# Kernel tuning notes

Hardware: AMD Instinct MI355X
Metric: run time of the kernel (lower is better)

The kernel has to match this reference:

```python
import jax, jax.numpy as jnp
import numpy as np

HIDDEN = 2048
N_HEADS = 16
N_KV_HEADS = 4
HEAD_DIM = HIDDEN // N_HEADS  # 128
ROPE_THETA = 10000.0
BATCH = 2
SEQ = 2048


def setup_inputs() -> dict:
    key = jax.random.key(0)
    k1, k2, k3, k4, k5 = jax.random.split(key, 5)
    s = 0.02
    return {
        "hidden_states": jax.random.normal(k1, (BATCH, SEQ, HIDDEN), dtype=jnp.float32),
        "attention_mask": jnp.zeros((BATCH, 1, 1, SEQ), dtype=jnp.float32),
        "Wq": jax.random.normal(k2, (HIDDEN, N_HEADS * HEAD_DIM), dtype=jnp.float32) * s,
        "Wk": jax.random.normal(k3, (HIDDEN, N_KV_HEADS * HEAD_DIM), dtype=jnp.float32) * s,
        "Wv": jax.random.normal(k4, (HIDDEN, N_KV_HEADS * HEAD_DIM), dtype=jnp.float32) * s,
        "Wo": jax.random.normal(k5, (N_HEADS * HEAD_DIM, HIDDEN), dtype=jnp.float32) * s,
    }


def _rope_cos_sin(seq_len, dtype):
    inv_freq = 1.0 / (ROPE_THETA ** (jnp.arange(0, HEAD_DIM, 2, dtype=jnp.float32) / HEAD_DIM))
    t = jnp.arange(seq_len, dtype=jnp.float32)
    freqs = t[:, None] * inv_freq[None, :]            # [S, D/2]
    emb = jnp.concatenate([freqs, freqs], axis=-1)    # [S, D]
    cos = jnp.cos(emb)[None, None, :, :].astype(dtype)  # [1,1,S,D]
    sin = jnp.sin(emb)[None, None, :, :].astype(dtype)
    return cos, sin


def _apply_rope(x, cos, sin):
    # x: [B,H,S,D]; faithful to torch code: rotated = cat((-x[...,1::2], x[...,::2]), -1)
    x1 = x[..., ::2]
    x2 = x[..., 1::2]
    rotated = jnp.concatenate([-x2, x1], axis=-1)
    return x * cos + rotated * sin


def reference(hidden_states, attention_mask, Wq, Wk, Wv, Wo):
    B, S, _ = hidden_states.shape
    scale = HEAD_DIM ** -0.5

    q = (hidden_states @ Wq).reshape(B, S, N_HEADS, HEAD_DIM).transpose(0, 2, 1, 3)      # [B,H,S,D]
    k = (hidden_states @ Wk).reshape(B, S, N_KV_HEADS, HEAD_DIM).transpose(0, 2, 1, 3)   # [B,KV,S,D]
    v = (hidden_states @ Wv).reshape(B, S, N_KV_HEADS, HEAD_DIM).transpose(0, 2, 1, 3)

    cos, sin = _rope_cos_sin(S, hidden_states.dtype)
    q = _apply_rope(q, cos, sin)
    k = _apply_rope(k, cos, sin)

    rep = N_HEADS // N_KV_HEADS
    k = jnp.repeat(k, rep, axis=1)  # [B,H,S,D]
    v = jnp.repeat(v, rep, axis=1)

    scores = jnp.einsum("bhqd,bhkd->bhqk", q, k) * scale  # [B,H,S,S]
    causal = jnp.tril(jnp.ones((S, S), dtype=bool))[None, None]
    scores = jnp.where(causal, scores, -jnp.inf)
    scores = scores + attention_mask  # additive float mask, broadcast [B,1,1,S]

    attn = jax.nn.softmax(scores, axis=-1)
    out = jnp.einsum("bhqk,bhkd->bhqd", attn, v)           # [B,H,S,D]
    out = out.transpose(0, 2, 1, 3).reshape(B, S, N_HEADS * HEAD_DIM)
    return out @ Wo
```

## Files before the change

### kernel.cpp

```cpp
#include <hip/hip_runtime.h>
#include <hip/hip_bf16.h>

#define BATCH 2
#define SEQ   2048
#define NH    16
#define NKV   4
#define HD    128
#define KDIM  2048
#define MROWS 4096
#define NQKV  3072

typedef __attribute__((ext_vector_type(8))) short  s16x8;
typedef __attribute__((ext_vector_type(4))) short  s16x4;
typedef __attribute__((ext_vector_type(4))) float  f32x4;
typedef __attribute__((ext_vector_type(8))) __bf16 b16x8;

__device__ __forceinline__ unsigned short f2bf(float f) {
  __hip_bfloat16 h = __float2bfloat16(f);
  return *reinterpret_cast<unsigned short*>(&h);
}
__device__ __forceinline__ float bf2f(unsigned short h) {
  union { unsigned int u; float f; } x; x.u = ((unsigned int)h) << 16;
  return x.f;
}

__device__ __forceinline__ f32x4 MFMA16(s16x8 a, s16x8 b, f32x4 c) {
  return __builtin_amdgcn_mfma_f32_16x16x32_bf16(
      __builtin_bit_cast(b16x8, a), __builtin_bit_cast(b16x8, b), c, 0, 0, 0);
}

__device__ __forceinline__ void gload_lds16(const void* g, void* lds) {
  __builtin_amdgcn_global_load_lds(
      (const __attribute__((address_space(1))) void*)g,
      (__attribute__((address_space(3))) void*)lds, 16, 0, 0);
}

__global__ __launch_bounds__(256) void transpose_convert(
    const float* __restrict__ W, unsigned short* __restrict__ WT, int Kd, int Nd) {
  __shared__ float tile[32][33];
  int n0 = blockIdx.x * 32, k0 = blockIdx.y * 32;
  int tx = threadIdx.x & 31, ty = threadIdx.x >> 5;
#pragma unroll
  for (int i = 0; i < 4; ++i)
    tile[ty + i * 8][tx] = W[(size_t)(k0 + ty + i * 8) * Nd + n0 + tx];
  __syncthreads();
#pragma unroll
  for (int i = 0; i < 4; ++i)
    WT[(size_t)(n0 + ty + i * 8) * Kd + k0 + tx] = f2bf(tile[tx][ty + i * 8]);
}

__global__ __launch_bounds__(256) void conv_bf16(
    const float* __restrict__ X, unsigned short* __restrict__ Y) {
  int i = blockIdx.x * 256 + threadIdx.x;
  const float4 a = ((const float4*)X)[2 * i];
  const float4 b = ((const float4*)X)[2 * i + 1];
  s16x8 o;
  o[0] = (short)f2bf(a.x); o[1] = (short)f2bf(a.y);
  o[2] = (short)f2bf(a.z); o[3] = (short)f2bf(a.w);
  o[4] = (short)f2bf(b.x); o[5] = (short)f2bf(b.y);
  o[6] = (short)f2bf(b.z); o[7] = (short)f2bf(b.w);
  ((s16x8*)Y)[i] = o;
}

__global__ __launch_bounds__(256) void rope_table_kernel(float* __restrict__ tbl) {
  int i = blockIdx.x * 256 + threadIdx.x;
  int s = i >> 6, j = i & 63;
  float inv = powf(10000.0f, -(float)(2 * j) * (1.0f / 128.0f));
  float f = (float)s * inv;
  tbl[2 * i]     = cosf(f);
  tbl[2 * i + 1] = sinf(f);
}

__global__ __launch_bounds__(256) void gemm_qkv(
    const unsigned short* __restrict__ A, const unsigned short* __restrict__ BT,
    unsigned short* __restrict__ Qo, unsigned short* __restrict__ Ko,
    unsigned short* __restrict__ Vo) {
  __shared__ __align__(16) unsigned short la[128][32];
  __shared__ __align__(16) unsigned short lb[128][32];
  int tid = threadIdx.x, lane = tid & 63, w = tid >> 6;
  int m0 = blockIdx.y * 128, n0 = blockIdx.x * 128;
  int wr = (w >> 1) * 64, wc = (w & 1) * 64;
  int fr = lane & 15, kg = (lane >> 4) * 8, rg = (lane >> 4) * 4;
  f32x4 acc[4][4] = {};
  for (int kt = 0; kt < KDIM; kt += 32) {
    __syncthreads();
#pragma unroll
    for (int i = 0; i < 2; ++i) {
      int idx = tid + i * 256;
      int row = idx >> 2, seg = idx & 3;
      gload_lds16(A + (size_t)(m0 + row) * KDIM + kt + seg * 8,
                  (char*)la + (size_t)(i * 256 + w * 64) * 16);
      gload_lds16(BT + (size_t)(n0 + row) * KDIM + kt + seg * 8,
                  (char*)lb + (size_t)(i * 256 + w * 64) * 16);
    }
    __syncthreads();
    s16x8 af[4], bf[4];
#pragma unroll
    for (int mi = 0; mi < 4; ++mi) af[mi] = *(const s16x8*)(&la[wr + mi * 16 + fr][kg]);
#pragma unroll
    for (int ni = 0; ni < 4; ++ni) bf[ni] = *(const s16x8*)(&lb[wc + ni * 16 + fr][kg]);
#pragma unroll
    for (int mi = 0; mi < 4; ++mi)
#pragma unroll
      for (int ni = 0; ni < 4; ++ni) acc[mi][ni] = MFMA16(af[mi], bf[ni], acc[mi][ni]);
  }
  int rbase = m0 + wr + rg;
#pragma unroll
  for (int ni = 0; ni < 4; ++ni) {
    int gn = n0 + wc + ni * 16 + fr;
    if (gn < 2048) {
      int hh = gn >> 7, d = gn & 127;
#pragma unroll
      for (int mi = 0; mi < 4; ++mi)
#pragma unroll
        for (int r = 0; r < 4; ++r) {
          int grow = rbase + mi * 16 + r;
          int bb = grow >> 11, ss = grow & 2047;
          Qo[((size_t)(bb * NH + hh) * SEQ + ss) * HD + d] = f2bf(acc[mi][ni][r]);
        }
    } else if (gn < 2560) {
      int c = gn - 2048, kvh = c >> 7, d = c & 127;
#pragma unroll
      for (int mi = 0; mi < 4; ++mi)
#pragma unroll
        for (int r = 0; r < 4; ++r) {
          int grow = rbase + mi * 16 + r;
          int bb = grow >> 11, ss = grow & 2047;
          Ko[((size_t)(bb * NKV + kvh) * SEQ + ss) * HD + d] = f2bf(acc[mi][ni][r]);
        }
    } else {
      int c = gn - 2560, kvh = c >> 7, d = c & 127;
#pragma unroll
      for (int mi = 0; mi < 4; ++mi) {
        int grow0 = rbase + mi * 16;
        int bb = grow0 >> 11, ss = grow0 & 2047;
        s16x4 pk;
#pragma unroll
        for (int r = 0; r < 4; ++r) pk[r] = (short)f2bf(acc[mi][ni][r]);
        *(s16x4*)(Vo + ((size_t)(bb * NKV + kvh) * HD + d) * SEQ + ss) = pk;
      }
    }
  }
}

__global__ __launch_bounds__(256) void gemm_out(
    const unsigned short* __restrict__ A, const unsigned short* __restrict__ BT,
    float* __restrict__ C) {
  __shared__ __align__(16) unsigned short la[128][32];
  __shared__ __align__(16) unsigned short lb[128][32];
  int tid = threadIdx.x, lane = tid & 63, w = tid >> 6;
  int m0 = blockIdx.y * 128, n0 = blockIdx.x * 128;
  int wr = (w >> 1) * 64, wc = (w & 1) * 64;
  int fr = lane & 15, kg = (lane >> 4) * 8, rg = (lane >> 4) * 4;
  f32x4 acc[4][4] = {};
  for (int kt = 0; kt < KDIM; kt += 32) {
    __syncthreads();
#pragma unroll
    for (int i = 0; i < 2; ++i) {
      int idx = tid + i * 256;
      int row = idx >> 2, seg = idx & 3;
      gload_lds16(A + (size_t)(m0 + row) * KDIM + kt + seg * 8,
                  (char*)la + (size_t)(i * 256 + w * 64) * 16);
      gload_lds16(BT + (size_t)(n0 + row) * KDIM + kt + seg * 8,
                  (char*)lb + (size_t)(i * 256 + w * 64) * 16);
    }
    __syncthreads();
    s16x8 af[4], bf[4];
#pragma unroll
    for (int mi = 0; mi < 4; ++mi) af[mi] = *(const s16x8*)(&la[wr + mi * 16 + fr][kg]);
#pragma unroll
    for (int ni = 0; ni < 4; ++ni) bf[ni] = *(const s16x8*)(&lb[wc + ni * 16 + fr][kg]);
#pragma unroll
    for (int mi = 0; mi < 4; ++mi)
#pragma unroll
      for (int ni = 0; ni < 4; ++ni) acc[mi][ni] = MFMA16(af[mi], bf[ni], acc[mi][ni]);
  }
  int rbase = m0 + wr + rg;
#pragma unroll
  for (int ni = 0; ni < 4; ++ni) {
    int gn = n0 + wc + ni * 16 + fr;
#pragma unroll
    for (int mi = 0; mi < 4; ++mi)
#pragma unroll
      for (int r = 0; r < 4; ++r)
        C[(size_t)(rbase + mi * 16 + r) * 2048 + gn] = acc[mi][ni][r];
  }
}

__global__ __launch_bounds__(256) void rope2(
    unsigned short* __restrict__ X, const float* __restrict__ tbl) {
  __shared__ __align__(16) unsigned short xs[32][136];
  int tid = threadIdx.x;
  size_t r0 = (size_t)blockIdx.x * 32;
#pragma unroll
  for (int i = 0; i < 2; ++i) {
    int idx = tid + i * 256;
    int pr = idx >> 4, seg = idx & 15;
    *(s16x8*)(&xs[pr][seg * 8]) = *(const s16x8*)(X + (r0 + pr) * 128 + seg * 8);
  }
  __syncthreads();
  int pr = tid >> 3, jb = (tid & 7) * 8;
  size_t row = r0 + pr;
  int s = (int)(row & (SEQ - 1));
  s16x8 o0, o1;
#pragma unroll
  for (int j0 = 0; j0 < 8; ++j0) {
    int j = jb + j0;
    float c  = tbl[(s * 64 + j) * 2];
    float sn = tbl[(s * 64 + j) * 2 + 1];
    float xj   = bf2f(xs[pr][j]);
    float xj64 = bf2f(xs[pr][j + 64]);
    float x2j  = bf2f(xs[pr][2 * j]);
    float x2j1 = bf2f(xs[pr][2 * j + 1]);
    o0[j0] = (short)f2bf(xj * c - x2j1 * sn);
    o1[j0] = (short)f2bf(xj64 * c + x2j * sn);
  }
  unsigned short* xp = X + row * 128;
  *(s16x8*)(xp + jb)      = o0;
  *(s16x8*)(xp + 64 + jb) = o1;
}

__global__ __launch_bounds__(256, 2) void attn_fwd(
    const unsigned short* __restrict__ Q, const unsigned short* __restrict__ K,
    const unsigned short* __restrict__ VT, const float* __restrict__ mask,
    unsigned short* __restrict__ O) {
  __shared__ __align__(16) unsigned short kt_[2][64][136];
  __shared__ __align__(16) unsigned short vt_[128][72];
  __shared__ __align__(16) unsigned short pt_[4][32][40];

  int tid = threadIdx.x, lane = tid & 63, w = tid >> 6;
  int l = blockIdx.x;
  int grp = l & 7, slot = l >> 3;
  int hloc = slot & 3, qt = 15 - (slot >> 2);
  int b = grp >> 2, kvh = grp & 3, h = kvh * 4 + hloc;
  int qbase = qt * 128;
  int fr = lane & 15, g = lane >> 4, kg = g * 8, rg = g * 4;
  int qw = qbase + w * 32;

  const unsigned short* Qb = Q + (size_t)(b * NH + h) * SEQ * HD;
  const unsigned short* Kb = K + (size_t)(b * NKV + kvh) * SEQ * HD;
  const unsigned short* Vb = VT + (size_t)(b * NKV + kvh) * HD * SEQ;
  const float* mb = mask + (size_t)b * SEQ;

  s16x8 aq[2][4];
#pragma unroll
  for (int nq = 0; nq < 2; ++nq)
#pragma unroll
    for (int dc = 0; dc < 4; ++dc)
      aq[nq][dc] = *(const s16x8*)(Qb + (size_t)(qw + nq * 16 + fr) * HD + dc * 32 + kg);

  int krow = tid >> 4, kpos = (tid & 15) * 8;

  f32x4 oacc[2][8] = {};
  float m_r[2] = {-3e38f, -3e38f}, l_r[2] = {0.f, 0.f};
  const float sc = 0.08838834764831845f;
  int ntiles = 2 * qt + 2;

  s16x8 kreg[4], vreg[4];
#pragma unroll
  for (int i = 0; i < 4; ++i)
    kreg[i] = *(const s16x8*)(Kb + (size_t)(krow + i * 16) * HD + kpos);
#pragma unroll
  for (int i = 0; i < 4; ++i) {
    int c = tid + 256 * i;
    vreg[i] = *(const s16x8*)(Vb + (size_t)(c >> 3) * SEQ + (c & 7) * 8);
  }
#pragma unroll
  for (int i = 0; i < 4; ++i)
    *(s16x8*)(&kt_[0][krow + i * 16][kpos]) = kreg[i];
  __syncthreads();

  int cur = 0;
  for (int t = 0; t < ntiles; ++t) {
    int kv0 = t * 64;
    bool active = (kv0 <= qw + 31);

#pragma unroll
    for (int i = 0; i < 4; ++i) {
      int c = tid + 256 * i;
      *(s16x8*)(&vt_[c >> 3][(c & 7) * 8]) = vreg[i];
    }
    if (t + 1 < ntiles) {
#pragma unroll
      for (int i = 0; i < 4; ++i)
        kreg[i] = *(const s16x8*)(Kb + (size_t)(kv0 + 64 + krow + i * 16) * HD + kpos);
    }

    f32x4 sf[4][2];
    if (active) {
      __builtin_amdgcn_s_setprio(1);
#pragma unroll
      for (int mk = 0; mk < 4; ++mk) {
        s16x8 ak[4];
#pragma unroll
        for (int dc = 0; dc < 4; ++dc)
          ak[dc] = *(const s16x8*)(&kt_[cur][mk * 16 + fr][dc * 32 + kg]);
        sf[mk][0] = f32x4{0.f, 0.f, 0.f, 0.f};
        sf[mk][1] = f32x4{0.f, 0.f, 0.f, 0.f};
#pragma unroll
        for (int nq = 0; nq < 2; ++nq)
#pragma unroll
          for (int dc = 0; dc < 4; ++dc)
            sf[mk][nq] = MFMA16(ak[dc], aq[nq][dc], sf[mk][nq]);
      }
      __builtin_amdgcn_s_setprio(0);

#pragma unroll
      for (int mk = 0; mk < 4; ++mk) {
        float4 mv = *(const float4*)(mb + kv0 + mk * 16 + rg);
        float mvr[4] = {mv.x, mv.y, mv.z, mv.w};
#pragma unroll
        for (int nq = 0; nq < 2; ++nq)
#pragma unroll
          for (int r = 0; r < 4; ++r) {
            int kv = kv0 + mk * 16 + rg + r;
            int q  = qw + nq * 16 + fr;
            float v = sf[mk][nq][r] * sc + mvr[r];
            sf[mk][nq][r] = (kv <= q) ? v : -3e38f;
          }
      }

#pragma unroll
      for (int nq = 0; nq < 2; ++nq) {
        float pm = -3e38f;
#pragma unroll
        for (int mk = 0; mk < 4; ++mk)
#pragma unroll
          for (int r = 0; r < 4; ++r) pm = fmaxf(pm, sf[mk][nq][r]);
        pm = fmaxf(pm, __shfl_xor(pm, 16, 64));
        pm = fmaxf(pm, __shfl_xor(pm, 32, 64));
        if (!__all(pm - m_r[nq] <= 8.0f)) {
          float mo = m_r[nq];
          float mn = fmaxf(mo, pm);
          float al = __expf(mo - mn);
          m_r[nq] = mn;
          l_r[nq] *= al;
#pragma unroll
          for (int r = 0; r < 4; ++r) {
            float ar = __shfl(al, rg + r, 16);
#pragma unroll
            for (int od = 0; od < 8; ++od) oacc[nq][od][r] *= ar;
          }
        }
        float rs = 0.f;
#pragma unroll
        for (int mk = 0; mk < 4; ++mk)
#pragma unroll
          for (int r = 0; r < 4; ++r) {
            float p = __expf(sf[mk][nq][r] - m_r[nq]);
            sf[mk][nq][r] = p;
            rs += p;
          }
        rs += __shfl_xor(rs, 16, 64);
        rs += __shfl_xor(rs, 32, 64);
        l_r[nq] += rs;
      }
    }

    if (t + 1 < ntiles) {
#pragma unroll
      for (int i = 0; i < 4; ++i)
        *(s16x8*)(&kt_[cur ^ 1][krow + i * 16][kpos]) = kreg[i];
    }
    __syncthreads();

    if (t + 1 < ntiles) {
#pragma unroll
      for (int i = 0; i < 4; ++i) {
        int c = tid + 256 * i;
        vreg[i] = *(const s16x8*)(Vb + (size_t)(c >> 3) * SEQ + kv0 + 64 + (c & 7) * 8);
      }
    }
    if (active) {
#pragma unroll
      for (int kk = 0; kk < 2; ++kk) {
#pragma unroll
        for (int nq = 0; nq < 2; ++nq)
#pragma unroll
          for (int mh = 0; mh < 2; ++mh) {
            int mk = kk * 2 + mh;
            s16x4 pk;
#pragma unroll
            for (int r = 0; r < 4; ++r) pk[r] = (short)f2bf(sf[mk][nq][r]);
            *(s16x4*)(&pt_[w][nq * 16 + fr][mh * 16 + rg]) = pk;
          }
        s16x8 ap[2];
#pragma unroll
        for (int nq = 0; nq < 2; ++nq)
          ap[nq] = *(const s16x8*)(&pt_[w][nq * 16 + fr][kg]);
        __builtin_amdgcn_s_setprio(1);
#pragma unroll
        for (int od = 0; od < 8; ++od) {
          s16x8 bv = *(const s16x8*)(&vt_[od * 16 + fr][kk * 32 + kg]);
#pragma unroll
          for (int nq = 0; nq < 2; ++nq)
            oacc[nq][od] = MFMA16(ap[nq], bv, oacc[nq][od]);
        }
        __builtin_amdgcn_s_setprio(0);
      }
    }
    __syncthreads();
    cur ^= 1;
  }

  int bS = b * SEQ;
#pragma unroll
  for (int nq = 0; nq < 2; ++nq) {
    float iv = 1.0f / l_r[nq];
    float ivr[4];
#pragma unroll
    for (int r = 0; r < 4; ++r) ivr[r] = __shfl(iv, rg + r, 16);
#pragma unroll
    for (int r = 0; r < 4; ++r) {
      unsigned short* op = O + (size_t)(bS + qw + nq * 16 + rg + r) * 2048 + h * 128 + fr;
#pragma unroll
      for (int od = 0; od < 8; ++od)
        op[od * 16] = f2bf(oacc[nq][od][r] * ivr[r]);
    }
  }
}

extern "C" void kernel_launch(void* const* d_in, const int* in_sizes, int n_in,
                              void* d_out, int out_size, void* d_ws, size_t ws_size,
                              hipStream_t stream) {
  const float* hidden = (const float*)d_in[0];
  const float* mask   = (const float*)d_in[1];
  const float* Wq     = (const float*)d_in[2];
  const float* Wk     = (const float*)d_in[3];
  const float* Wv     = (const float*)d_in[4];
  const float* Wo     = (const float*)d_in[5];
  float* out = (float*)d_out;

  char* ws = (char*)d_ws;
  unsigned short* BT  = (unsigned short*)(ws);
  unsigned short* WoT = (unsigned short*)(ws + 12582912);
  unsigned short* Qb  = (unsigned short*)(ws + 20971520);
  unsigned short* Kb  = (unsigned short*)(ws + 37748736);
  unsigned short* VT  = (unsigned short*)(ws + 41943040);
  unsigned short* AO  = (unsigned short*)(ws + 46137344);
  float*          tbl = (float*)(ws + 62914560);
  unsigned short* Ab  = AO;

  conv_bf16<<<MROWS * KDIM / (256 * 8), 256, 0, stream>>>(hidden, Ab);
  transpose_convert<<<dim3(64, 64), 256, 0, stream>>>(Wq, BT, KDIM, 2048);
  transpose_convert<<<dim3(16, 64), 256, 0, stream>>>(Wk, BT + (size_t)2048 * KDIM, KDIM, 512);
  transpose_convert<<<dim3(16, 64), 256, 0, stream>>>(Wv, BT + (size_t)2560 * KDIM, KDIM, 512);
  transpose_convert<<<dim3(64, 64), 256, 0, stream>>>(Wo, WoT, KDIM, 2048);
  rope_table_kernel<<<512, 256, 0, stream>>>(tbl);

  gemm_qkv<<<dim3(NQKV / 128, MROWS / 128), 256, 0, stream>>>(Ab, BT, Qb, Kb, VT);
  rope2<<<(BATCH * NH * SEQ) / 32, 256, 0, stream>>>(Qb, tbl);
  rope2<<<(BATCH * NKV * SEQ) / 32, 256, 0, stream>>>(Kb, tbl);
  attn_fwd<<<dim3(512), 256, 0, stream>>>(Qb, Kb, VT, mask, AO);
  gemm_out<<<dim3(2048 / 128, MROWS / 128), 256, 0, stream>>>(AO, WoT, out);
}
```

Baseline: 234.6 us.

## Shrink attention query tile to 64, read V directly from global, use exp2

```diff
diff --git a/kernel.cpp b/kernel.cpp
--- a/kernel.cpp
+++ b/kernel.cpp
@@ -220,51 +220,44 @@
   *(s16x8*)(xp + 64 + jb) = o1;
 }
 
-__global__ __launch_bounds__(256, 2) void attn_fwd(
+__global__ __launch_bounds__(256, 4) void attn_fwd(
     const unsigned short* __restrict__ Q, const unsigned short* __restrict__ K,
     const unsigned short* __restrict__ VT, const float* __restrict__ mask,
     unsigned short* __restrict__ O) {
   __shared__ __align__(16) unsigned short kt_[2][64][136];
-  __shared__ __align__(16) unsigned short vt_[128][72];
-  __shared__ __align__(16) unsigned short pt_[4][32][40];
+  __shared__ __align__(16) unsigned short pt_[4][16][36];
 
   int tid = threadIdx.x, lane = tid & 63, w = tid >> 6;
   int l = blockIdx.x;
   int grp = l & 7, slot = l >> 3;
-  int hloc = slot & 3, qt = 15 - (slot >> 2);
+  int hloc = slot & 3, qt = 31 - (slot >> 2);
   int b = grp >> 2, kvh = grp & 3, h = kvh * 4 + hloc;
-  int qbase = qt * 128;
+  int qbase = qt * 64;
   int fr = lane & 15, g = lane >> 4, kg = g * 8, rg = g * 4;
-  int qw = qbase + w * 32;
+  int qw = qbase + w * 16;
 
   const unsigned short* Qb = Q + (size_t)(b * NH + h) * SEQ * HD;
   const unsigned short* Kb = K + (size_t)(b * NKV + kvh) * SEQ * HD;
   const unsigned short* Vb = VT + (size_t)(b * NKV + kvh) * HD * SEQ;
   const float* mb = mask + (size_t)b * SEQ;
 
-  s16x8 aq[2][4];
-#pragma unroll
-  for (int nq = 0; nq < 2; ++nq)
-#pragma unroll
-    for (int dc = 0; dc < 4; ++dc)
-      aq[nq][dc] = *(const s16x8*)(Qb + (size_t)(qw + nq * 16 + fr) * HD + dc * 32 + kg);
+  s16x8 aq[4];
+#pragma unroll
+  for (int dc = 0; dc < 4; ++dc)
+    aq[dc] = *(const s16x8*)(Qb + (size_t)(qw + fr) * HD + dc * 32 + kg);
 
   int krow = tid >> 4, kpos = (tid & 15) * 8;
 
-  f32x4 oacc[2][8] = {};
-  float m_r[2] = {-3e38f, -3e38f}, l_r[2] = {0.f, 0.f};
-  const float sc = 0.08838834764831845f;
-  int ntiles = 2 * qt + 2;
-
-  s16x8 kreg[4], vreg[4];
+  f32x4 oacc[8] = {};
+  float m_r = -3e38f, l_r = 0.f;
+  const float sc2 = 0.12751744584812722f;
+  const float L2E = 1.44269504088896f;
+  int ntiles = qt + 1;
+
+  s16x8 kreg[4];
 #pragma unroll
   for (int i = 0; i < 4; ++i)
     kreg[i] = *(const s16x8*)(Kb + (size_t)(krow + i * 16) * HD + kpos);
-#pragma unroll
-  for (int i = 0; i < 4; ++i) {
-    int c = tid + 256 * i;
-    vreg[i] = *(const s16x8*)(Vb + (size_t)(c >> 3) * SEQ + (c & 7) * 8);
-  }
 #pragma unroll
   for (int i = 0; i < 4; ++i)
     *(s16x8*)(&kt_[0][krow + i * 16][kpos]) = kreg[i];
@@ -273,20 +266,16 @@
   int cur = 0;
   for (int t = 0; t < ntiles; ++t) {
     int kv0 = t * 64;
-    bool active = (kv0 <= qw + 31);
-
-#pragma unroll
-    for (int i = 0; i < 4; ++i) {
-      int c = tid + 256 * i;
-      *(s16x8*)(&vt_[c >> 3][(c & 7) * 8]) = vreg[i];
-    }
+    bool active = (kv0 <= qw + 15);
+    bool diag   = (kv0 + 63 > qw);
+
     if (t + 1 < ntiles) {
 #pragma unroll
       for (int i = 0; i < 4; ++i)
         kreg[i] = *(const s16x8*)(Kb + (size_t)(kv0 + 64 + krow + i * 16) * HD + kpos);
     }
 
-    f32x4 sf[4][2];
+    f32x4 sf[4];
     if (active) {
       __builtin_amdgcn_s_setprio(1);
 #pragma unroll
@@ -295,66 +284,64 @@
 #pragma unroll
         for (int dc = 0; dc < 4; ++dc)
           ak[dc] = *(const s16x8*)(&kt_[cur][mk * 16 + fr][dc * 32 + kg]);
-        sf[mk][0] = f32x4{0.f, 0.f, 0.f, 0.f};
-        sf[mk][1] = f32x4{0.f, 0.f, 0.f, 0.f};
-#pragma unroll
-        for (int nq = 0; nq < 2; ++nq)
-#pragma unroll
-          for (int dc = 0; dc < 4; ++dc)
-            sf[mk][nq] = MFMA16(ak[dc], aq[nq][dc], sf[mk][nq]);
+        sf[mk] = f32x4{0.f, 0.f, 0.f, 0.f};
+#pragma unroll
+        for (int dc = 0; dc < 4; ++dc)
+          sf[mk] = MFMA16(ak[dc], aq[dc], sf[mk]);
       }
       __builtin_amdgcn_s_setprio(0);
 
 #pragma unroll
       for (int mk = 0; mk < 4; ++mk) {
         float4 mv = *(const float4*)(mb + kv0 + mk * 16 + rg);
-        float mvr[4] = {mv.x, mv.y, mv.z, mv.w};
-#pragma unroll
-        for (int nq = 0; nq < 2; ++nq)
+        float mvr[4] = {mv.x * L2E, mv.y * L2E, mv.z * L2E, mv.w * L2E};
+        if (diag) {
 #pragma unroll
           for (int r = 0; r < 4; ++r) {
             int kv = kv0 + mk * 16 + rg + r;
-            int q  = qw + nq * 16 + fr;
-            float v = sf[mk][nq][r] * sc + mvr[r];
-            sf[mk][nq][r] = (kv <= q) ? v : -3e38f;
+            int q  = qw + fr;
+            float v = sf[mk][r] * sc2 + mvr[r];
+            sf[mk][r] = (kv <= q) ? v : -3e38f;
           }
+        } else {
+#pragma unroll
+          for (int r = 0; r < 4; ++r)
+            sf[mk][r] = sf[mk][r] * sc2 + mvr[r];
+        }
       }
 
-#pragma unroll
-      for (int nq = 0; nq < 2; ++nq) {
-        float pm = -3e38f;
-#pragma unroll
-        for (int mk = 0; mk < 4; ++mk)
-#pragma unroll
-          for (int r = 0; r < 4; ++r) pm = fmaxf(pm, sf[mk][nq][r]);
-        pm = fmaxf(pm, __shfl_xor(pm, 16, 64));
-        pm = fmaxf(pm, __shfl_xor(pm, 32, 64));
-        if (!__all(pm - m_r[nq] <= 8.0f)) {
-          float mo = m_r[nq];
-          float mn = fmaxf(mo, pm);
-          float al = __expf(mo - mn);
-          m_r[nq] = mn;
-          l_r[nq] *= al;
-#pragma unroll
-          for (int r = 0; r < 4; ++r) {
-            float ar = __shfl(al, rg + r, 16);
-#pragma unroll
-            for (int od = 0; od < 8; ++od) oacc[nq][od][r] *= ar;
-          }
-        }
-        float rs = 0.f;
-#pragma unroll
-        for (int mk = 0; mk < 4; ++mk)
-#pragma unroll
-          for (int r = 0; r < 4; ++r) {
-            float p = __expf(sf[mk][nq][r] - m_r[nq]);
-            sf[mk][nq][r] = p;
-            rs += p;
-          }
-        rs += __shfl_xor(rs, 16, 64);
-        rs += __shfl_xor(rs, 32, 64);
-        l_r[nq] += rs;
+      float pm = -3e38f;
+#pragma unroll
+      for (int mk = 0; mk < 4; ++mk)
+#pragma unroll
+        for (int r = 0; r < 4; ++r) pm = fmaxf(pm, sf[mk][r]);
+      pm = fmaxf(pm, __shfl_xor(pm, 16, 64));
+      pm = fmaxf(pm, __shfl_xor(pm, 32, 64));
+      if (!__all(pm - m_r <= 8.0f)) {
+        float mo = m_r;
+        float mn = fmaxf(mo, pm);
+        float al = exp2f(mo - mn);
+        m_r = mn;
+        l_r *= al;
+#pragma unroll
+        for (int r = 0; r < 4; ++r) {
+          float ar = __shfl(al, rg + r, 16);
+#pragma unroll
+          for (int od = 0; od < 8; ++od) oacc[od][r] *= ar;
+        }
       }
+      float rs = 0.f;
+#pragma unroll
+      for (int mk = 0; mk < 4; ++mk)
+#pragma unroll
+        for (int r = 0; r < 4; ++r) {
+          float p = exp2f(sf[mk][r] - m_r);
+          sf[mk][r] = p;
+          rs += p;
+        }
+      rs += __shfl_xor(rs, 16, 64);
+      rs += __shfl_xor(rs, 32, 64);
+      l_r += rs;
     }
 
     if (t + 1 < ntiles) {
@@ -364,59 +351,41 @@
     }
     __syncthreads();
 
-    if (t + 1 < ntiles) {
-#pragma unroll
-      for (int i = 0; i < 4; ++i) {
-        int c = tid + 256 * i;
-        vreg[i] = *(const s16x8*)(Vb + (size_t)(c >> 3) * SEQ + kv0 + 64 + (c & 7) * 8);
-      }
-    }
     if (active) {
 #pragma unroll
       for (int kk = 0; kk < 2; ++kk) {
 #pragma unroll
-        for (int nq = 0; nq < 2; ++nq)
-#pragma unroll
-          for (int mh = 0; mh < 2; ++mh) {
-            int mk = kk * 2 + mh;
-            s16x4 pk;
-#pragma unroll
-            for (int r = 0; r < 4; ++r) pk[r] = (short)f2bf(sf[mk][nq][r]);
-            *(s16x4*)(&pt_[w][nq * 16 + fr][mh * 16 + rg]) = pk;
-          }
-        s16x8 ap[2];
-#pragma unroll
-        for (int nq = 0; nq < 2; ++nq)
-          ap[nq] = *(const s16x8*)(&pt_[w][nq * 16 + fr][kg]);
+        for (int mh = 0; mh < 2; ++mh) {
+          int mk = kk * 2 + mh;
+          s16x4 pk;
+#pragma unroll
+          for (int r = 0; r < 4; ++r) pk[r] = (short)f2bf(sf[mk][r]);
+          *(s16x4*)(&pt_[w][fr][mh * 16 + rg]) = pk;
+        }
+        s16x8 ap = *(const s16x8*)(&pt_[w][fr][kg]);
         __builtin_amdgcn_s_setprio(1);
 #pragma unroll
         for (int od = 0; od < 8; ++od) {
-          s16x8 bv = *(const s16x8*)(&vt_[od * 16 + fr][kk * 32 + kg]);
-#pragma unroll
-          for (int nq = 0; nq < 2; ++nq)
-            oacc[nq][od] = MFMA16(ap[nq], bv, oacc[nq][od]);
+          s16x8 bv = *(const s16x8*)(Vb + (size_t)(od * 16 + fr) * SEQ + kv0 + kk * 32 + kg);
+          oacc[od] = MFMA16(ap, bv, oacc[od]);
         }
         __builtin_amdgcn_s_setprio(0);
       }
     }
-    __syncthreads();
     cur ^= 1;
   }
 
   int bS = b * SEQ;
-#pragma unroll
-  for (int nq = 0; nq < 2; ++nq) {
-    float iv = 1.0f / l_r[nq];
-    float ivr[4];
-#pragma unroll
-    for (int r = 0; r < 4; ++r) ivr[r] = __shfl(iv, rg + r, 16);
-#pragma unroll
-    for (int r = 0; r < 4; ++r) {
-      unsigned short* op = O + (size_t)(bS + qw + nq * 16 + rg + r) * 2048 + h * 128 + fr;
-#pragma unroll
-      for (int od = 0; od < 8; ++od)
-        op[od * 16] = f2bf(oacc[nq][od][r] * ivr[r]);
-    }
+  float iv = 1.0f / l_r;
+  float ivr[4];
+#pragma unroll
+  for (int r = 0; r < 4; ++r) ivr[r] = __shfl(iv, rg + r, 16);
+#pragma unroll
+  for (int r = 0; r < 4; ++r) {
+    unsigned short* op = O + (size_t)(bS + qw + rg + r) * 2048 + h * 128 + fr;
+#pragma unroll
+    for (int od = 0; od < 8; ++od)
+      op[od * 16] = f2bf(oacc[od][r] * ivr[r]);
   }
 }
 
@@ -451,6 +420,6 @@
   gemm_qkv<<<dim3(NQKV / 128, MROWS / 128), 256, 0, stream>>>(Ab, BT, Qb, Kb, VT);
   rope2<<<(BATCH * NH * SEQ) / 32, 256, 0, stream>>>(Qb, tbl);
   rope2<<<(BATCH * NKV * SEQ) / 32, 256, 0, stream>>>(Kb, tbl);
-  attn_fwd<<<dim3(512), 256, 0, stream>>>(Qb, Kb, VT, mask, AO);
+  attn_fwd<<<dim3(1024), 256, 0, stream>>>(Qb, Kb, VT, mask, AO);
   gemm_out<<<dim3(2048 / 128, MROWS / 128), 256, 0, stream>>>(AO, WoT, out);
 }
```

After: 359.7 us. 53.3% more time.
